# Kernel optimization log

Hardware: AMD Instinct MI355X
Metric: run time of the kernel (lower is better)

Reference implementation:

```python
import jax, jax.numpy as jnp
import numpy as np

K = 4
TEMPERATURE = 34.0
OUT_CH = 256
KSIZE = 3
PAD = 1


def setup_inputs() -> dict:
    key = jax.random.key(0)
    ks = jax.random.split(key, 6)
    B, C, H, W = 16, 256, 56, 56
    hidden = int(C * 0.25) + 1  # 65
    x = jax.random.normal(ks[0], (B, C, H, W), dtype=jnp.float32)
    w_fc1 = jax.random.normal(ks[1], (hidden, C), dtype=jnp.float32) * (2.0 / C) ** 0.5
    w_fc2 = jax.random.normal(ks[2], (K, hidden), dtype=jnp.float32) * (2.0 / hidden) ** 0.5
    b_fc2 = jnp.zeros((K,), dtype=jnp.float32)
    weight = jax.random.normal(ks[3], (OUT_CH, C, KSIZE, KSIZE), dtype=jnp.float32) * 0.05
    bias = jax.random.normal(ks[4], (K, OUT_CH), dtype=jnp.float32) * 0.01
    return {"x": x, "w_fc1": w_fc1, "w_fc2": w_fc2, "b_fc2": b_fc2,
            "weight": weight, "bias": bias}


def _attention(x, w_fc1, w_fc2, b_fc2):
    pooled = x.mean(axis=(2, 3))                     # [B, C] adaptive avgpool(1)
    h = jax.nn.relu(pooled @ w_fc1.T)                # 1x1 conv == linear
    raw = h @ w_fc2.T + b_fc2                        # [B, K]
    # gradient_approximation: hard one-hot fwd, softmax(x/T) bwd (straight-through)
    hard = jax.nn.one_hot(jnp.argmax(raw, axis=1), raw.shape[1], dtype=raw.dtype)
    soft = jax.nn.softmax(raw / TEMPERATURE, axis=1)
    att = jax.lax.stop_gradient(hard - soft) + soft
    return att, raw


def _quantize_banks(weight):
    # WDoReFaQuantizer with 'modified' scheme, bits 2..K+1, STE on the round step
    w = weight.reshape(-1)
    t = jnp.tanh(w)
    xq = t / jnp.max(jnp.abs(t))
    xq = (xq + 1.0) * 0.5                            # in [0, 1]
    banks = []
    for bit in range(2, 2 + K):
        a = float(1 << bit)
        q = jnp.minimum(jnp.floor(a * xq), a - 1.0) / a
        q = jax.lax.stop_gradient(q - xq) + xq       # STE: identity backward
        banks.append(q * 2.0 - 1.0)
    return jnp.stack(banks)                          # [K, O*C*k*k]


def reference(x, w_fc1, w_fc2, b_fc2, weight, bias):
    B, C, H, W = x.shape
    att, raw = _attention(x, w_fc1, w_fc2, b_fc2)    # [B, K], [B, K]
    wq = _quantize_banks(weight)                     # [K, N]
    agg_w = (att @ wq).reshape(B, OUT_CH, C, KSIZE, KSIZE)
    agg_b = att @ bias                               # [B, OUT_CH]

    def conv1(xi, wi):  # xi: [C,H,W], wi: [O,C,k,k]
        return jax.lax.conv_general_dilated(
            xi[None], wi, window_strides=(1, 1),
            padding=[(PAD, PAD), (PAD, PAD)],
            dimension_numbers=("NCHW", "OIHW", "NCHW"))[0]

    out = jax.vmap(conv1)(x, agg_w) + agg_b[:, :, None, None]
    return (out, raw)
```

## Files before the change

### kernel.cpp

```cpp
#include <hip/hip_runtime.h>
#include <math.h>

#define NB 16
#define NC 256
#define NH 56
#define NW 56
#define NHW 3136
#define NHID 65
#define NK 4
#define NOC 256
#define WN 589824
#define OUT0 12845056

#define WS_POOLED 0
#define WS_KB     4096
#define WS_MAX    4112
#define WS_MAXP   4128
#define WS_WQF    8192
#define WQB_OFF   32768ul
#define XP_OFF    4751360ul
#define WS_NEED   32325632ul

typedef unsigned int u32;
typedef unsigned short u16;
typedef unsigned long long u64;
typedef __attribute__((ext_vector_type(8))) short s8v;
typedef __attribute__((ext_vector_type(16))) float f16v;

__device__ __forceinline__ u16 f2bf(float f) {
    union { float f; u32 u; } v; v.f = f;
    u32 u = v.u;
    return (u16)((u + 0x7fffu + ((u >> 16) & 1u)) >> 16);
}

__device__ __forceinline__ void gload_lds16(const void* g, void* l) {
    __builtin_amdgcn_global_load_lds((const __attribute__((address_space(1))) u32*)g,
                                     (__attribute__((address_space(3))) u32*)l, 16, 0, 0);
}


__global__ __launch_bounds__(256) void k_prep(const float* __restrict__ x,
                                              const float* __restrict__ w,
                                              float* __restrict__ ws,
                                              float* __restrict__ scratch) {
    const int tid = threadIdx.x;
    if (blockIdx.x >= 224) {
        int j = blockIdx.x - 224;
        float m = 0.f;
        for (int i = j * 256 + tid; i < WN; i += 65536)
            m = fmaxf(m, fabsf(tanhf(w[i])));
        for (int off = 32; off > 0; off >>= 1) m = fmaxf(m, __shfl_down(m, off, 64));
        __shared__ float part[4];
        int lane = tid & 63, wv = tid >> 6;
        if (lane == 0) part[wv] = m;
        __syncthreads();
        if (tid == 0)
            ws[WS_MAXP + j] = fmaxf(fmaxf(part[0], part[1]), fmaxf(part[2], part[3]));
        return;
    }
    const int b = blockIdx.x / 14, yg = blockIdx.x % 14;
    const int c16 = tid >> 4, q = tid & 15;
    __shared__ u16 Lbt[56 * 264];
    u16* xp = (u16*)((char*)ws + XP_OFF);

    float rs[16];
    #pragma unroll
    for (int i = 0; i < 16; ++i) rs[i] = 0.f;

    for (int ry = 0; ry < 4; ++ry) {
        int y = yg * 4 + ry;
        #pragma unroll
        for (int ci = 0; ci < 16; ++ci) {
            int c = ci * 16 + c16;
            float4 v = make_float4(0.f, 0.f, 0.f, 0.f);
            if (q < 14) {
                v = *(const float4*)(x + ((size_t)(b * 256 + c)) * NHW + (size_t)y * 56 + q * 4);
                Lbt[(q * 4 + 0) * 264 + c] = f2bf(v.x);
                Lbt[(q * 4 + 1) * 264 + c] = f2bf(v.y);
                Lbt[(q * 4 + 2) * 264 + c] = f2bf(v.z);
                Lbt[(q * 4 + 3) * 264 + c] = f2bf(v.w);
            }
            rs[ci] += v.x + v.y + v.z + v.w;
        }
        __syncthreads();
        u64* rowp = (u64*)xp + (size_t)(b * 58 + y + 1) * (58 * 64);
        for (int idx = tid; idx < 58 * 64; idx += 256) {
            int col = idx >> 6, cp = idx & 63;
            u64 v = 0ull;
            if (col >= 1 && col <= 56)
                v = *(const u64*)(Lbt + (col - 1) * 264 + cp * 4);
            rowp[idx] = v;
        }
        __syncthreads();
    }
    #pragma unroll
    for (int ci = 0; ci < 16; ++ci) {
        float s = rs[ci];
        s += __shfl_xor(s, 8, 16);
        s += __shfl_xor(s, 4, 16);
        s += __shfl_xor(s, 2, 16);
        s += __shfl_xor(s, 1, 16);
        if (q == 0)
            scratch[(size_t)(b * 256 + ci * 16 + c16) * 14 + yg] = s;
    }
    if (yg == 0 || yg == 13) {
        int row = (yg == 0) ? 0 : 57;
        u64* rowp = (u64*)xp + (size_t)(b * 58 + row) * (58 * 64);
        for (int idx = tid; idx < 58 * 64; idx += 256) rowp[idx] = 0ull;
    }
}

__global__ __launch_bounds__(256) void k_mid(const float* __restrict__ w_fc1,
                                             const float* __restrict__ w_fc2,
                                             const float* __restrict__ b_fc2,
                                             const float* __restrict__ w,
                                             float* __restrict__ ws,
                                             const float* __restrict__ scratch,
                                             float* __restrict__ out_raw) {
    const int tid = threadIdx.x;
    if (blockIdx.x < 16) {
        const int b = blockIdx.x;
        __shared__ float pl[NC];
        __shared__ float hs[NHID];
        __shared__ float raws[NK];
        float p = 0.f;
        #pragma unroll
        for (int yg = 0; yg < 14; ++yg)
            p += scratch[(size_t)(b * 256 + tid) * 14 + yg];
        pl[tid] = p * (1.0f / NHW);
        __syncthreads();
        if (tid < NHID) {
            float s = 0.f;
            for (int c = 0; c < NC; ++c) s = fmaf(pl[c], w_fc1[tid * NC + c], s);
            hs[tid] = fmaxf(s, 0.f);
        }
        __syncthreads();
        if (tid < NK) {
            float s = b_fc2[tid];
            for (int j = 0; j < NHID; ++j) s = fmaf(hs[j], w_fc2[tid * NHID + j], s);
            raws[tid] = s;
            out_raw[b * NK + tid] = s;
        }
        __syncthreads();
        if (tid == 0) {
            int best = 0;
            for (int k = 1; k < NK; ++k) if (raws[k] > raws[best]) best = k;
            ((int*)(ws + WS_KB))[b] = best;
        }
        return;
    }
    __shared__ float mred[4];
    float mv = ws[WS_MAXP + tid];
    for (int off = 32; off > 0; off >>= 1) mv = fmaxf(mv, __shfl_down(mv, off, 64));
    if ((tid & 63) == 0) mred[tid >> 6] = mv;
    __syncthreads();
    const float maxt = fmaxf(fmaxf(mred[0], mred[1]), fmaxf(mred[2], mred[3]));

    u16* wqp = (u16*)((char*)ws + WQB_OFF);
    int idx = (blockIdx.x - 16) * 256 + tid;
    int o = idx >> 7, c2 = idx & 127;
    int ch0 = c2 * 2;
    int cs = ch0 >> 5, cc = ch0 & 31;
    int ks2 = cc >> 4, hf = (cc >> 3) & 1, j = cc & 7;
    int n = o & 31, ot = o >> 5;
    const float* wp = w + ((size_t)o * 256 + ch0) * 9;
    float t0[9], t1[9];
    #pragma unroll
    for (int t = 0; t < 9; ++t) t0[t] = tanhf(wp[t]);
    #pragma unroll
    for (int t = 0; t < 9; ++t) t1[t] = tanhf(wp[9 + t]);
    #pragma unroll
    for (int bank = 0; bank < 4; ++bank) {
        float a = (float)(4 << bank);
        #pragma unroll
        for (int tap = 0; tap < 9; ++tap) {
            float xq0 = (t0[tap] / maxt + 1.f) * 0.5f;
            float xq1 = (t1[tap] / maxt + 1.f) * 0.5f;
            float q0 = fminf(floorf(a * xq0), a - 1.f) / a * 2.f - 1.f;
            float q1 = fminf(floorf(a * xq1), a - 1.f) / a * 2.f - 1.f;
            u32 pk = (u32)f2bf(q0) | ((u32)f2bf(q1) << 16);
            size_t off16 = ((((size_t)((bank * 8 + ot) * 8 + cs)) * 18 + tap * 2 + ks2) * 64
                            + hf * 32 + n) * 8 + j;
            *(u32*)(wqp + off16) = pk;
        }
    }
}

__global__ __launch_bounds__(512, 2) void k_conv_mfma(const float* __restrict__ bias,
                                                      const float* __restrict__ ws_f,
                                                      float* __restrict__ out) {
    const int half = blockIdx.x;
    const int r0 = blockIdx.y * 8;
    const int b  = blockIdx.z;
    const int tid = threadIdx.x;
    const int wv = tid >> 6, lane = tid & 63;
    const int ot = wv & 3, nh = wv >> 2;
    const int n = lane & 31, hf = lane >> 5;
    const int kb = ((const int*)(ws_f + WS_KB))[b];
    const u16* wqp = (const u16*)((const char*)ws_f + WQB_OFF);
    const u16* xp  = (const u16*)((const char*)ws_f + XP_OFF);

    __shared__ __align__(16) u16 Xl[2][20480];

    int bofs[7];
    #pragma unroll
    for (int t = 0; t < 7; ++t) {
        int p = nh * 224 + 32 * t + n, pr = p / 56, pc = p - pr * 56;
        bofs[t] = pr * 4096 + hf * 1024 + pc * 16;
    }
    const int colc = (lane < 58) ? lane : 57;
    const u16* xsrc = xp + (((size_t)(b * 58 + r0)) * 58 + colc) * 256;
    const u16* abase = wqp + (size_t)((kb * 8 + half * 4 + ot) * 8) * (18 * 64 * 8);

    f16v acc[7];
    #pragma unroll
    for (int t = 0; t < 7; ++t) acc[t] = (f16v)0.f;

    #pragma unroll
    for (int i = 0; i < 5; ++i) {
        int seg = wv * 5 + i;
        gload_lds16(xsrc + (size_t)(seg >> 2) * (58 * 256) + (seg & 3) * 8,
                    (void*)(&Xl[0][seg * 512]));
    }
    __syncthreads();

    #pragma unroll 1
    for (int cs = 0; cs < 8; ++cs) {
        int pb = cs & 1;
        if (cs < 7) {
            int c0n = (cs + 1) * 32;
            #pragma unroll
            for (int i = 0; i < 5; ++i) {
                int seg = wv * 5 + i;
                gload_lds16(xsrc + (size_t)(seg >> 2) * (58 * 256) + (seg & 3) * 8 + c0n,
                            (void*)(&Xl[pb ^ 1][seg * 512]));
            }
        }
        const u16* ap = abase + (size_t)cs * (18 * 64 * 8);
        s8v a[18];
        #pragma unroll
        for (int f = 0; f < 18; ++f)
            a[f] = *(const s8v*)(ap + (size_t)(f * 64 + lane) * 8);
        const char* XB = (const char*)&Xl[pb][0];
        #pragma unroll
        for (int r = 0; r < 3; ++r)
            #pragma unroll
            for (int s = 0; s < 3; ++s)
                #pragma unroll
                for (int ks = 0; ks < 2; ++ks) {
                    const int coff = r * 4096 + ks * 2048 + s * 16;
                    s8v af = a[(r * 3 + s) * 2 + ks];
                    #pragma unroll
                    for (int t = 0; t < 7; ++t) {
                        s8v bf = *(const s8v*)(XB + bofs[t] + coff);
                        acc[t] = __builtin_amdgcn_mfma_f32_32x32x16_bf16(af, bf, acc[t], 0, 0, 0);
                    }
                }
        __syncthreads();
    }

    #pragma unroll
    for (int t = 0; t < 7; ++t) {
        int p = nh * 224 + 32 * t + n, pr = p / 56, pc = p - pr * 56;
        float* op = out + (size_t)b * 256 * NHW + (size_t)(r0 + pr) * 56 + pc;
        #pragma unroll
        for (int reg = 0; reg < 16; ++reg) {
            int m = (reg & 3) + 8 * (reg >> 2) + 4 * hf;
            int o = half * 128 + ot * 32 + m;
            op[(size_t)o * NHW] = acc[t][reg] + bias[kb * NOC + o];
        }
    }
}


__global__ __launch_bounds__(256) void k_pool(const float* __restrict__ x,
                                              float* __restrict__ ws) {
    int plane = blockIdx.x;
    const float* p = x + (size_t)plane * NHW;
    float s = 0.f;
    for (int i = threadIdx.x; i < NHW; i += 256) s += p[i];
    for (int off = 32; off > 0; off >>= 1) s += __shfl_down(s, off, 64);
    __shared__ float part[4];
    int lane = threadIdx.x & 63, wv = threadIdx.x >> 6;
    if (lane == 0) part[wv] = s;
    __syncthreads();
    if (threadIdx.x == 0)
        ws[WS_POOLED + plane] = part[0] + part[1] + part[2] + part[3];
}

__global__ __launch_bounds__(256) void k_fc(const float* __restrict__ w_fc1,
                                            const float* __restrict__ w_fc2,
                                            const float* __restrict__ b_fc2,
                                            float* __restrict__ ws,
                                            float* __restrict__ out_raw) {
    __shared__ float pl[NB * NC];
    __shared__ float hs[NB][NHID];
    __shared__ float raws[NB][NK];
    for (int i = threadIdx.x; i < NB * NC; i += 256)
        pl[i] = ws[WS_POOLED + i] * (1.0f / NHW);
    __syncthreads();
    for (int idx = threadIdx.x; idx < NB * NHID; idx += 256) {
        int b = idx / NHID, j = idx % NHID;
        float s = 0.f;
        for (int c = 0; c < NC; ++c) s = fmaf(pl[b * NC + c], w_fc1[j * NC + c], s);
        hs[b][j] = fmaxf(s, 0.f);
    }
    __syncthreads();
    if (threadIdx.x < NB * NK) {
        int b = threadIdx.x / NK, k = threadIdx.x % NK;
        float s = b_fc2[k];
        for (int j = 0; j < NHID; ++j) s = fmaf(hs[b][j], w_fc2[k * NHID + j], s);
        raws[b][k] = s;
        out_raw[b * NK + k] = s;
    }
    __syncthreads();
    if (threadIdx.x < NB) {
        int best = 0;
        for (int k = 1; k < NK; ++k)
            if (raws[threadIdx.x][k] > raws[threadIdx.x][best]) best = k;
        ((int*)(ws + WS_KB))[threadIdx.x] = best;
    }
}

__global__ __launch_bounds__(256) void k_maxtanh(const float* __restrict__ w,
                                                 float* __restrict__ ws) {
    float m = 0.f;
    for (int i = blockIdx.x * 256 + threadIdx.x; i < WN; i += gridDim.x * 256)
        m = fmaxf(m, fabsf(tanhf(w[i])));
    for (int off = 32; off > 0; off >>= 1) m = fmaxf(m, __shfl_down(m, off, 64));
    __shared__ float part[4];
    int lane = threadIdx.x & 63, wv = threadIdx.x >> 6;
    if (lane == 0) part[wv] = m;
    __syncthreads();
    if (threadIdx.x == 0) {
        float t = fmaxf(fmaxf(part[0], part[1]), fmaxf(part[2], part[3]));
        atomicMax((unsigned int*)ws + WS_MAX, __float_as_uint(t));
    }
}

__global__ __launch_bounds__(256) void k_quant(const float* __restrict__ w,
                                               float* __restrict__ ws) {
    float maxt = __uint_as_float(((const unsigned int*)ws)[WS_MAX]);
    float* wqf = ws + WS_WQF;
    for (int i = blockIdx.x * 256 + threadIdx.x; i < WN; i += gridDim.x * 256) {
        float t = tanhf(w[i]);
        float xq = (t / maxt + 1.0f) * 0.5f;
        #pragma unroll
        for (int k = 0; k < NK; ++k) {
            float a = (float)(4 << k);
            float q = fminf(floorf(a * xq), a - 1.0f) / a;
            wqf[(size_t)k * WN + i] = q * 2.0f - 1.0f;
        }
    }
}

__global__ __launch_bounds__(256) void k_conv(const float* __restrict__ x,
                                              const float* __restrict__ bias,
                                              const float* __restrict__ ws,
                                              float* __restrict__ out) {
    const int o_base = blockIdx.x * 16;
    const int row_base = blockIdx.y * 7;
    const int b = blockIdx.z;
    const int tid = threadIdx.x;
    const int w = tid & 63;
    const int og = tid >> 6;
    const int wc = (w < 56) ? w : 55;
    const int kb = ((const int*)(ws + WS_KB))[b];
    const float* wqf = ws + WS_WQF + (size_t)kb * WN;

    __shared__ float Xl[8][9][58];
    __shared__ float Wl[16][72];

    float acc[4][7];
    #pragma unroll
    for (int i = 0; i < 4; ++i)
        #pragma unroll
        for (int j = 0; j < 7; ++j) acc[i][j] = 0.f;

    for (int c0 = 0; c0 < NC; c0 += 8) {
        for (int idx = tid; idx < 1152; idx += 256) {
            int o = idx / 72, rem = idx - o * 72;
            Wl[o][rem] = wqf[(size_t)(o_base + o) * 2304 + c0 * 9 + rem];
        }
        for (int idx = tid; idx < 4176; idx += 256) {
            int c = idx / 522, rem = idx - c * 522;
            int ly = rem / 58, lx = rem - ly * 58;
            int gy = row_base - 1 + ly, gx = lx - 1;
            float v = 0.f;
            if (gy >= 0 && gy < NH && (unsigned)gx < (unsigned)NW)
                v = x[(((size_t)b * NC + c0 + c) * NH + gy) * NW + gx];
            Xl[c][ly][lx] = v;
        }
        __syncthreads();
        #pragma unroll 1
        for (int c = 0; c < 8; ++c) {
            float xv[9][3];
            #pragma unroll
            for (int ly = 0; ly < 9; ++ly)
                #pragma unroll
                for (int s = 0; s < 3; ++s)
                    xv[ly][s] = Xl[c][ly][wc + s];
            float wvv[4][9];
            #pragma unroll
            for (int i = 0; i < 4; ++i)
                #pragma unroll
                for (int t = 0; t < 9; ++t)
                    wvv[i][t] = Wl[og * 4 + i][c * 9 + t];
            #pragma unroll
            for (int i = 0; i < 4; ++i)
                #pragma unroll
                for (int j = 0; j < 7; ++j)
                    #pragma unroll
                    for (int r = 0; r < 3; ++r)
                        #pragma unroll
                        for (int s = 0; s < 3; ++s)
                            acc[i][j] = fmaf(wvv[i][r * 3 + s], xv[j + r][s], acc[i][j]);
        }
        __syncthreads();
    }

    if (w < 56) {
        #pragma unroll
        for (int i = 0; i < 4; ++i) {
            int o = o_base + og * 4 + i;
            float bb = bias[kb * NOC + o];
            #pragma unroll
            for (int j = 0; j < 7; ++j)
                out[(((size_t)b * NOC + o) * NH + (row_base + j)) * NW + w] = acc[i][j] + bb;
        }
    }
}

extern "C" void kernel_launch(void* const* d_in, const int* in_sizes, int n_in,
                              void* d_out, int out_size, void* d_ws, size_t ws_size,
                              hipStream_t stream) {
    const float* x      = (const float*)d_in[0];
    const float* w_fc1  = (const float*)d_in[1];
    const float* w_fc2  = (const float*)d_in[2];
    const float* b_fc2  = (const float*)d_in[3];
    const float* weight = (const float*)d_in[4];
    const float* bias   = (const float*)d_in[5];
    float* out = (float*)d_out;
    float* ws  = (float*)d_ws;

    if (ws_size >= WS_NEED) {
        hipLaunchKernelGGL(k_prep, dim3(480), dim3(256), 0, stream, x, weight, ws, out);
        hipLaunchKernelGGL(k_mid, dim3(144), dim3(256), 0, stream,
                           w_fc1, w_fc2, b_fc2, weight, ws, out, out + OUT0);
        hipLaunchKernelGGL(k_conv_mfma, dim3(2, 7, 16), dim3(512), 0, stream, bias, ws, out);
    } else {
        hipLaunchKernelGGL(k_pool, dim3(NB * NC), dim3(256), 0, stream, x, ws);
        hipLaunchKernelGGL(k_fc, dim3(1), dim3(256), 0, stream,
                           w_fc1, w_fc2, b_fc2, ws, out + OUT0);
        hipLaunchKernelGGL(k_maxtanh, dim3(256), dim3(256), 0, stream, weight, ws);
        hipLaunchKernelGGL(k_quant, dim3(512), dim3(256), 0, stream, weight, ws);
        hipLaunchKernelGGL(k_conv, dim3(16, 8, NB), dim3(256), 0, stream, x, bias, ws, out);
    }
}
```

Before: 215.6 us.

## Retile conv to 64-channel blocks with 4 waves and restructure prep transpose

The conv kernel now launches 4x7x16 blocks of 256 threads. Each block covers 64 output channels, and each wave computes two 32-row A tiles over 3-4 pixel tiles, so every LDS B fragment feeds two MFMAs. A fragments are loaded per kernel row instead of all 18 at once, which lowers register pressure. The prep kernel switches to one wave per channel with coalesced scalar loads and a full wave reduction per row, writing 56 partial sums per channel, and changes the LDS pitch to 260. The waves get uneven work (4 vs 3 tiles), and more blocks each reload the same activation tile.

```diff
diff --git a/kernel.cpp b/kernel.cpp
--- a/kernel.cpp
+++ b/kernel.cpp
@@ -38,6 +38,8 @@
                                      (__attribute__((address_space(3))) u32*)l, 16, 0, 0);
 }
 
+
+#define LBT_P 260
 
 __global__ __launch_bounds__(256) void k_prep(const float* __restrict__ x,
                                               const float* __restrict__ w,
@@ -59,28 +61,24 @@
         return;
     }
     const int b = blockIdx.x / 14, yg = blockIdx.x % 14;
-    const int c16 = tid >> 4, q = tid & 15;
-    __shared__ u16 Lbt[56 * 264];
+    const int lane = tid & 63, wv = tid >> 6;
+    __shared__ u16 Lbt[56 * LBT_P];
     u16* xp = (u16*)((char*)ws + XP_OFF);
 
-    float rs[16];
-    #pragma unroll
-    for (int i = 0; i < 16; ++i) rs[i] = 0.f;
-
     for (int ry = 0; ry < 4; ++ry) {
-        int y = yg * 4 + ry;
-        #pragma unroll
-        for (int ci = 0; ci < 16; ++ci) {
-            int c = ci * 16 + c16;
-            float4 v = make_float4(0.f, 0.f, 0.f, 0.f);
-            if (q < 14) {
-                v = *(const float4*)(x + ((size_t)(b * 256 + c)) * NHW + (size_t)y * 56 + q * 4);
-                Lbt[(q * 4 + 0) * 264 + c] = f2bf(v.x);
-                Lbt[(q * 4 + 1) * 264 + c] = f2bf(v.y);
-                Lbt[(q * 4 + 2) * 264 + c] = f2bf(v.z);
-                Lbt[(q * 4 + 3) * 264 + c] = f2bf(v.w);
-            }
-            rs[ci] += v.x + v.y + v.z + v.w;
+        const int y = yg * 4 + ry;
+        if (ry) __syncthreads();
+        #pragma unroll 4
+        for (int cg = 0; cg < 64; ++cg) {
+            int c = cg * 4 + wv;
+            float v = 0.f;
+            if (lane < 56)
+                v = x[((size_t)(b * 256 + c)) * NHW + (size_t)y * 56 + lane];
+            if (lane < 56) Lbt[lane * LBT_P + c] = f2bf(v);
+            float s = v;
+            for (int off = 32; off > 0; off >>= 1) s += __shfl_down(s, off, 64);
+            if (lane == 0)
+                scratch[((size_t)(b * 256 + c)) * 56 + y] = s;
         }
         __syncthreads();
         u64* rowp = (u64*)xp + (size_t)(b * 58 + y + 1) * (58 * 64);
@@ -88,20 +86,9 @@
             int col = idx >> 6, cp = idx & 63;
             u64 v = 0ull;
             if (col >= 1 && col <= 56)
-                v = *(const u64*)(Lbt + (col - 1) * 264 + cp * 4);
+                v = *(const u64*)(Lbt + (col - 1) * LBT_P + cp * 4);
             rowp[idx] = v;
         }
-        __syncthreads();
-    }
-    #pragma unroll
-    for (int ci = 0; ci < 16; ++ci) {
-        float s = rs[ci];
-        s += __shfl_xor(s, 8, 16);
-        s += __shfl_xor(s, 4, 16);
-        s += __shfl_xor(s, 2, 16);
-        s += __shfl_xor(s, 1, 16);
-        if (q == 0)
-            scratch[(size_t)(b * 256 + ci * 16 + c16) * 14 + yg] = s;
     }
     if (yg == 0 || yg == 13) {
         int row = (yg == 0) ? 0 : 57;
@@ -124,9 +111,8 @@
         __shared__ float hs[NHID];
         __shared__ float raws[NK];
         float p = 0.f;
-        #pragma unroll
-        for (int yg = 0; yg < 14; ++yg)
-            p += scratch[(size_t)(b * 256 + tid) * 14 + yg];
+        for (int y = 0; y < 56; ++y)
+            p += scratch[((size_t)(b * 256 + tid)) * 56 + y];
         pl[tid] = p * (1.0f / NHW);
         __syncthreads();
         if (tid < NHID) {
@@ -186,39 +172,43 @@
     }
 }
 
-__global__ __launch_bounds__(512, 2) void k_conv_mfma(const float* __restrict__ bias,
+__global__ __launch_bounds__(256, 2) void k_conv_mfma(const float* __restrict__ bias,
                                                       const float* __restrict__ ws_f,
                                                       float* __restrict__ out) {
-    const int half = blockIdx.x;
+    const int oq = blockIdx.x;
     const int r0 = blockIdx.y * 8;
     const int b  = blockIdx.z;
     const int tid = threadIdx.x;
     const int wv = tid >> 6, lane = tid & 63;
-    const int ot = wv & 3, nh = wv >> 2;
     const int n = lane & 31, hf = lane >> 5;
+    const int noff  = (wv < 2) ? wv * 4 : 8 + (wv - 2) * 3;
+    const int ntile = (wv < 2) ? 4 : 3;
     const int kb = ((const int*)(ws_f + WS_KB))[b];
     const u16* wqp = (const u16*)((const char*)ws_f + WQB_OFF);
     const u16* xp  = (const u16*)((const char*)ws_f + XP_OFF);
 
     __shared__ __align__(16) u16 Xl[2][20480];
 
-    int bofs[7];
-    #pragma unroll
-    for (int t = 0; t < 7; ++t) {
-        int p = nh * 224 + 32 * t + n, pr = p / 56, pc = p - pr * 56;
+    int bofs[4];
+    #pragma unroll
+    for (int t = 0; t < 4; ++t) {
+        int p = (noff + t) * 32 + n;
+        if (t >= ntile) p = n;
+        int pr = p / 56, pc = p - pr * 56;
         bofs[t] = pr * 4096 + hf * 1024 + pc * 16;
     }
     const int colc = (lane < 58) ? lane : 57;
     const u16* xsrc = xp + (((size_t)(b * 58 + r0)) * 58 + colc) * 256;
-    const u16* abase = wqp + (size_t)((kb * 8 + half * 4 + ot) * 8) * (18 * 64 * 8);
-
-    f16v acc[7];
-    #pragma unroll
-    for (int t = 0; t < 7; ++t) acc[t] = (f16v)0.f;
-
-    #pragma unroll
-    for (int i = 0; i < 5; ++i) {
-        int seg = wv * 5 + i;
+    const u16* ab0 = wqp + (size_t)((kb * 8 + oq * 2 + 0) * 8) * (18 * 64 * 8);
+    const u16* ab1 = wqp + (size_t)((kb * 8 + oq * 2 + 1) * 8) * (18 * 64 * 8);
+
+    f16v acc0[4], acc1[4];
+    #pragma unroll
+    for (int t = 0; t < 4; ++t) { acc0[t] = (f16v)0.f; acc1[t] = (f16v)0.f; }
+
+    #pragma unroll
+    for (int i = 0; i < 10; ++i) {
+        int seg = wv * 10 + i;
         gload_lds16(xsrc + (size_t)(seg >> 2) * (58 * 256) + (seg & 3) * 8,
                     (void*)(&Xl[0][seg * 512]));
     }
@@ -230,46 +220,53 @@
         if (cs < 7) {
             int c0n = (cs + 1) * 32;
             #pragma unroll
-            for (int i = 0; i < 5; ++i) {
-                int seg = wv * 5 + i;
+            for (int i = 0; i < 10; ++i) {
+                int seg = wv * 10 + i;
                 gload_lds16(xsrc + (size_t)(seg >> 2) * (58 * 256) + (seg & 3) * 8 + c0n,
                             (void*)(&Xl[pb ^ 1][seg * 512]));
             }
         }
-        const u16* ap = abase + (size_t)cs * (18 * 64 * 8);
-        s8v a[18];
-        #pragma unroll
-        for (int f = 0; f < 18; ++f)
-            a[f] = *(const s8v*)(ap + (size_t)(f * 64 + lane) * 8);
+        const u16* ap0 = ab0 + (size_t)cs * (18 * 64 * 8);
+        const u16* ap1 = ab1 + (size_t)cs * (18 * 64 * 8);
         const char* XB = (const char*)&Xl[pb][0];
         #pragma unroll
-        for (int r = 0; r < 3; ++r)
+        for (int r = 0; r < 3; ++r) {
+            s8v a0[6], a1[6];
+            #pragma unroll
+            for (int j = 0; j < 6; ++j) {
+                a0[j] = *(const s8v*)(ap0 + (size_t)((r * 6 + j) * 64 + lane) * 8);
+                a1[j] = *(const s8v*)(ap1 + (size_t)((r * 6 + j) * 64 + lane) * 8);
+            }
             #pragma unroll
             for (int s = 0; s < 3; ++s)
                 #pragma unroll
                 for (int ks = 0; ks < 2; ++ks) {
                     const int coff = r * 4096 + ks * 2048 + s * 16;
-                    s8v af = a[(r * 3 + s) * 2 + ks];
                     #pragma unroll
-                    for (int t = 0; t < 7; ++t) {
-                        s8v bf = *(const s8v*)(XB + bofs[t] + coff);
-                        acc[t] = __builtin_amdgcn_mfma_f32_32x32x16_bf16(af, bf, acc[t], 0, 0, 0);
-                    }
+                    for (int t = 0; t < 4; ++t)
+                        if (t < ntile) {
+                            s8v bf = *(const s8v*)(XB + bofs[t] + coff);
+                            acc0[t] = __builtin_amdgcn_mfma_f32_32x32x16_bf16(a0[s * 2 + ks], bf, acc0[t], 0, 0, 0);
+                            acc1[t] = __builtin_amdgcn_mfma_f32_32x32x16_bf16(a1[s * 2 + ks], bf, acc1[t], 0, 0, 0);
+                        }
                 }
-        __syncthreads();
-    }
-
-    #pragma unroll
-    for (int t = 0; t < 7; ++t) {
-        int p = nh * 224 + 32 * t + n, pr = p / 56, pc = p - pr * 56;
-        float* op = out + (size_t)b * 256 * NHW + (size_t)(r0 + pr) * 56 + pc;
-        #pragma unroll
-        for (int reg = 0; reg < 16; ++reg) {
-            int m = (reg & 3) + 8 * (reg >> 2) + 4 * hf;
-            int o = half * 128 + ot * 32 + m;
-            op[(size_t)o * NHW] = acc[t][reg] + bias[kb * NOC + o];
-        }
-    }
+        }
+        __syncthreads();
+    }
+
+    #pragma unroll
+    for (int t = 0; t < 4; ++t)
+        if (t < ntile) {
+            int p = (noff + t) * 32 + n, pr = p / 56, pc = p - pr * 56;
+            float* op = out + (size_t)b * 256 * NHW + (size_t)(r0 + pr) * 56 + pc;
+            #pragma unroll
+            for (int reg = 0; reg < 16; ++reg) {
+                int m = (reg & 3) + 8 * (reg >> 2) + 4 * hf;
+                int o0 = oq * 64 + m;
+                op[(size_t)o0 * NHW] = acc0[t][reg] + bias[kb * NOC + o0];
+                op[(size_t)(o0 + 32) * NHW] = acc1[t][reg] + bias[kb * NOC + o0 + 32];
+            }
+        }
 }
 
 
@@ -447,7 +444,7 @@
         hipLaunchKernelGGL(k_prep, dim3(480), dim3(256), 0, stream, x, weight, ws, out);
         hipLaunchKernelGGL(k_mid, dim3(144), dim3(256), 0, stream,
                            w_fc1, w_fc2, b_fc2, weight, ws, out, out + OUT0);
-        hipLaunchKernelGGL(k_conv_mfma, dim3(2, 7, 16), dim3(512), 0, stream, bias, ws, out);
+        hipLaunchKernelGGL(k_conv_mfma, dim3(4, 7, 16), dim3(256), 0, stream, bias, ws, out);
     } else {
         hipLaunchKernelGGL(k_pool, dim3(NB * NC), dim3(256), 0, stream, x, ws);
         hipLaunchKernelGGL(k_fc, dim3(1), dim3(256), 0, stream,
```

Result: slower. 344.5 us (+59.8%).
